# Kernel tuning notes

Hardware: AMD Instinct MI355X
Metric: run time of the kernel (lower is better)

Reference implementation:

```python
import jax, jax.numpy as jnp
import numpy as np

MAX_DIM = 1024
VOCAB = 257
DEPTH = 6
Q_DIM = MAX_DIM // 4  # 256
EXP_DIMS = [1, 2, 4, 8, 16, 32, 64, 128]  # expander sizes: current_q doubles up to Q_DIM
BATCH, SEQ = 8, 4096


def qlinear(q, W):
    """Quaternion Hamilton-product linear.
    q: [..., in, 4] (last dim = r,i,j,k components), W: [4, out, in] (stacked r,i,j,k weights).
    Returns [..., out, 4].
    """
    # P[..., o, w, a] = F.linear(component_a, W_w)  -> all 16 small GEMMs in one einsum
    P = jnp.einsum('...ia,woi->...owa', q, W)
    Pr, Pi, Pj, Pk = P[..., 0, :], P[..., 1, :], P[..., 2, :], P[..., 3, :]  # each [..., out, 4]
    out_r = Pr[..., 0] - Pi[..., 1] - Pj[..., 2] - Pk[..., 3]
    out_i = Pi[..., 0] + Pr[..., 1] + Pk[..., 2] - Pj[..., 3]
    out_j = Pj[..., 0] - Pk[..., 1] + Pr[..., 2] + Pi[..., 3]
    out_k = Pk[..., 0] + Pj[..., 1] - Pi[..., 2] + Pr[..., 3]
    return jnp.stack([out_r, out_i, out_j, out_k], axis=-1)


def qnormalize(q):
    norm = jnp.linalg.norm(q, axis=-1, keepdims=True)
    return q / (norm + 1e-8)


def setup_inputs() -> dict:
    key = jax.random.key(0)
    ks = jax.random.split(key, 4 + len(EXP_DIMS))
    inp = {}
    inp['x'] = jax.random.randint(ks[0], (BATCH, SEQ), 0, VOCAB)
    inp['emb'] = jax.random.normal(ks[1], (VOCAB, 4), dtype=jnp.float32)
    for idx, cq in enumerate(EXP_DIMS):
        scale = cq ** (-0.5)
        inp[f'w_exp{idx}'] = jax.random.uniform(ks[2 + idx], (4, cq, cq), jnp.float32, -scale, scale)
    scale = Q_DIM ** (-0.5)
    inp['w_layers'] = jax.random.uniform(ks[-2], (DEPTH, 4, Q_DIM, Q_DIM), jnp.float32, -scale, scale)
    inp['w_head'] = jax.random.normal(ks[-1], (VOCAB, MAX_DIM), dtype=jnp.float32) * MAX_DIM ** (-0.5)
    return inp


def reference(x, emb, w_exp0, w_exp1, w_exp2, w_exp3, w_exp4, w_exp5, w_exp6, w_exp7,
              w_layers, w_head):
    q = emb[x][:, :, None, :]  # [B, S, 1, 4]
    for w in (w_exp0, w_exp1, w_exp2, w_exp3, w_exp4, w_exp5, w_exp6, w_exp7):
        delta = jnp.tanh(qlinear(q, w))
        q = jnp.concatenate([q + delta, q - delta], axis=2)  # doubles quaternion dim
    for d in range(DEPTH):
        q = qnormalize(qlinear(q, w_layers[d]))
    stability_loss = jnp.mean(jnp.abs(q[..., 0]))
    h_flat = q.reshape(x.shape[0], x.shape[1], -1)  # [B, S, MAX_DIM]
    logits = jnp.einsum('bsd,vd->bsv', h_flat, w_head)
    return (logits, stability_loss)
```

## Files before the change

kernel.cpp:

```cpp
#include <hip/hip_runtime.h>


typedef _Float16 f16x8 __attribute__((ext_vector_type(8)));
typedef float    f32x4 __attribute__((ext_vector_type(4)));

#define GL2LDS16(gp, lp) __builtin_amdgcn_global_load_lds(                     \
    (const __attribute__((address_space(1))) void*)(gp),                       \
    (__attribute__((address_space(3))) void*)(lp), 16, 0, 0)

__device__ __forceinline__ unsigned short f2h(float f) {
  union { _Float16 h; unsigned short u; } c;
  c.h = (_Float16)f;
  return c.u;
}
__device__ __forceinline__ float h2f(unsigned short u) {
  union { unsigned short u; _Float16 h; } c;
  c.u = u;
  return (float)c.h;
}

__global__ __launch_bounds__(256) void expand_ham(
    const float* __restrict__ w, unsigned short* __restrict__ out,
    int cq, int kbits, int total) {
  int id = blockIdx.x * 256 + threadIdx.x;
  if (id >= total) return;
  const int K = 1 << kbits;
  const int n = id >> kbits;
  const int k = id & (K - 1);
  float val = 0.f;
  if (n < 4 * cq) {
    const int o = n >> 2, a = n & 3, i = k >> 2, b = k & 3;
    const int   comp[4][4] = {{0,1,2,3},{1,0,3,2},{2,3,0,1},{3,2,1,0}};
    const float sgn [4][4] = {{1.f,-1.f,-1.f,-1.f},{1.f,1.f,1.f,-1.f},
                              {1.f,-1.f,1.f,1.f},{1.f,1.f,-1.f,1.f}};
    val = sgn[a][b] * w[comp[a][b] * cq * cq + o * cq + i];
  }
  out[id] = f2h(val);
}

__global__ __launch_bounds__(256) void conv_head(
    const float* __restrict__ wh, unsigned short* __restrict__ out) {
  int id = blockIdx.x * 256 + threadIdx.x;
  int v = id >> 10, k = id & 1023;
  out[id] = f2h(v < 257 ? wh[v * 1024 + k] : 0.f);
}

template <int CQ>
__device__ __forceinline__ void exp_step(float (&q)[16][4],
                                         const float* __restrict__ w) {
  float d[CQ][4];
#pragma unroll
  for (int o = 0; o < CQ; o++) {
    float pr = 0.f, pi = 0.f, pj = 0.f, pk = 0.f;
#pragma unroll
    for (int i = 0; i < CQ; i++) {
      const float wr = w[0 * CQ * CQ + o * CQ + i];
      const float wi = w[1 * CQ * CQ + o * CQ + i];
      const float wj = w[2 * CQ * CQ + o * CQ + i];
      const float wk = w[3 * CQ * CQ + o * CQ + i];
      const float qr = q[i][0], qi = q[i][1], qj = q[i][2], qk = q[i][3];
      pr += wr * qr - wi * qi - wj * qj - wk * qk;
      pi += wi * qr + wr * qi + wk * qj - wj * qk;
      pj += wj * qr - wk * qi + wr * qj + wi * qk;
      pk += wk * qr + wj * qi - wi * qj + wr * qk;
    }
    d[o][0] = tanhf(pr); d[o][1] = tanhf(pi);
    d[o][2] = tanhf(pj); d[o][3] = tanhf(pk);
  }
#pragma unroll
  for (int o = 0; o < CQ; o++)
#pragma unroll
    for (int a = 0; a < 4; a++) {
      const float dd = d[o][a], qq = q[o][a];
      q[o][a]      = qq + dd;
      q[CQ + o][a] = qq - dd;
    }
}

__global__ __launch_bounds__(256) void embed_expand(
    const int* __restrict__ x, const float* __restrict__ emb,
    const float* __restrict__ w0, const float* __restrict__ w1,
    const float* __restrict__ w2, const float* __restrict__ w3,
    unsigned short* __restrict__ out) {
  const int t = blockIdx.x * 256 + threadIdx.x;
  float q[16][4];
  const int v = x[t];
  const float4 e = *(const float4*)(emb + v * 4);
  q[0][0] = e.x; q[0][1] = e.y; q[0][2] = e.z; q[0][3] = e.w;
  exp_step<1>(q, w0);
  exp_step<2>(q, w1);
  exp_step<4>(q, w2);
  exp_step<8>(q, w3);
  ushort4* o4 = (ushort4*)(out + (size_t)t * 64);
#pragma unroll
  for (int c = 0; c < 16; c++) {
    ushort4 u;
    u.x = f2h(q[c][0]); u.y = f2h(q[c][1]);
    u.z = f2h(q[c][2]); u.w = f2h(q[c][3]);
    o4[c] = u;
  }
}

template <int EPI>
__global__ __launch_bounds__(256) void gemm_epi(
    const unsigned short* __restrict__ W,
    const unsigned short* __restrict__ Act,
    unsigned short* __restrict__ OutB, float* __restrict__ OutF,
    int K, int Nreal, int ldout) {
  __shared__ unsigned short WtL[128 * 32];
  __shared__ unsigned short WtH[128 * 32];
  __shared__ unsigned short AtL[128 * 32];
  __shared__ unsigned short AtH[128 * 32];

  const int tid  = threadIdx.x;
  const int wave = tid >> 6;
  const int lane = tid & 63;
  const int l15  = lane & 15;
  const int quad = lane >> 4;

  const int Gx = gridDim.x;
  const int L  = blockIdx.y * Gx + blockIdx.x;
  const int j  = L & 7;
  const int s  = L >> 3;
  const int nblock = (s % Gx) * 128;
  const int mblock = (32 * j + s / Gx) * 128;
  const int wn = (wave & 1) * 64;
  const int wm = (wave >> 1) * 64;

  f32x4 acc[4][4];
  const f32x4 zero = {0.f, 0.f, 0.f, 0.f};
#pragma unroll
  for (int a = 0; a < 4; a++)
#pragma unroll
    for (int b = 0; b < 4; b++) acc[a][b] = zero;

  const int row0 = tid >> 2;
  const int sub  = tid & 3;
  const unsigned short* gW0 = W   + (size_t)(nblock + row0)      * K + sub * 8;
  const unsigned short* gW1 = W   + (size_t)(nblock + row0 + 64) * K + sub * 8;
  const unsigned short* gA0 = Act + (size_t)(mblock + row0)      * K + sub * 8;
  const unsigned short* gA1 = Act + (size_t)(mblock + row0 + 64) * K + sub * 8;
  unsigned short* lWL0 = &WtL[wave * 512];
  unsigned short* lWL1 = &WtL[2048 + wave * 512];
  unsigned short* lWH0 = &WtH[wave * 512];
  unsigned short* lWH1 = &WtH[2048 + wave * 512];
  unsigned short* lAL0 = &AtL[wave * 512];
  unsigned short* lAL1 = &AtL[2048 + wave * 512];
  unsigned short* lAH0 = &AtH[wave * 512];
  unsigned short* lAH1 = &AtH[2048 + wave * 512];

  for (int kb = 0; kb < K; kb += 64) {
    GL2LDS16(gW0 + kb,      lWL0);
    GL2LDS16(gW1 + kb,      lWL1);
    GL2LDS16(gW0 + kb + 32, lWH0);
    GL2LDS16(gW1 + kb + 32, lWH1);
    GL2LDS16(gA0 + kb,      lAL0);
    GL2LDS16(gA1 + kb,      lAL1);
    GL2LDS16(gA0 + kb + 32, lAH0);
    GL2LDS16(gA1 + kb + 32, lAH1);
    __syncthreads();

    {
      f16x8 afr[4], bfr[4];
#pragma unroll
      for (int tn = 0; tn < 4; tn++)
        afr[tn] = *(const f16x8*)&WtL[(wn + tn * 16 + l15) * 32 + quad * 8];
#pragma unroll
      for (int tm = 0; tm < 4; tm++)
        bfr[tm] = *(const f16x8*)&AtL[(wm + tm * 16 + l15) * 32 + quad * 8];
#pragma unroll
      for (int tn = 0; tn < 4; tn++)
#pragma unroll
        for (int tm = 0; tm < 4; tm++)
          acc[tn][tm] = __builtin_amdgcn_mfma_f32_16x16x32_f16(
              afr[tn], bfr[tm], acc[tn][tm], 0, 0, 0);
    }
    {
      f16x8 afr[4], bfr[4];
#pragma unroll
      for (int tn = 0; tn < 4; tn++)
        afr[tn] = *(const f16x8*)&WtH[(wn + tn * 16 + l15) * 32 + quad * 8];
#pragma unroll
      for (int tm = 0; tm < 4; tm++)
        bfr[tm] = *(const f16x8*)&AtH[(wm + tm * 16 + l15) * 32 + quad * 8];
#pragma unroll
      for (int tn = 0; tn < 4; tn++)
#pragma unroll
        for (int tm = 0; tm < 4; tm++)
          acc[tn][tm] = __builtin_amdgcn_mfma_f32_16x16x32_f16(
              afr[tn], bfr[tm], acc[tn][tm], 0, 0, 0);
    }
    __syncthreads();
  }

#pragma unroll
  for (int tn = 0; tn < 4; tn++) {
    const int n = nblock + wn + tn * 16 + quad * 4;
    if (n < Nreal) {
#pragma unroll
      for (int tm = 0; tm < 4; tm++) {
        const int token = mblock + wm + tm * 16 + l15;
        const f32x4 v = acc[tn][tm];
        const unsigned short* ip = Act + (size_t)token * K + n;
        const float i0 = h2f(ip[0]), i1 = h2f(ip[1]);
        const float i2 = h2f(ip[2]), i3 = h2f(ip[3]);
        const float d0 = tanhf(v[0]), d1 = tanhf(v[1]);
        const float d2 = tanhf(v[2]), d3 = tanhf(v[3]);
        ushort4 up, um;
        up.x = f2h(i0 + d0); up.y = f2h(i1 + d1);
        up.z = f2h(i2 + d2); up.w = f2h(i3 + d3);
        um.x = f2h(i0 - d0); um.y = f2h(i1 - d1);
        um.z = f2h(i2 - d2); um.w = f2h(i3 - d3);
        *(ushort4*)&OutB[(size_t)token * ldout + n] = up;
        *(ushort4*)&OutB[(size_t)token * ldout + Nreal + n] = um;
      }
    }
  }
}

template <int EPI>
__global__ __launch_bounds__(512, 2) void gemm8p(
    const unsigned short* __restrict__ W,
    const unsigned short* __restrict__ Act,
    unsigned short* __restrict__ OutB, float* __restrict__ OutF,
    int K, int NW, int ldout) {
  __shared__ unsigned short S[65536];
  __shared__ float lsum[8];

  const int tid  = threadIdx.x;
  const int wave = tid >> 6;
  const int lane = tid & 63;
  const int l15  = lane & 15;
  const int quad = lane >> 4;
  const int wr   = wave >> 2;
  const int wc   = wave & 3;

  const int Gx = gridDim.x;
  const int L  = blockIdx.y * Gx + blockIdx.x;
  const int j  = L & 7;
  const int s  = L >> 3;
  const int mtile = j * (gridDim.y >> 3) + s / Gx;
  const int ntile = s % Gx;
  const int nblock = ntile * 256;
  const int mblock = mtile * 256;

  const int NT = K >> 5;

  f32x4 acc[8][4];
  const f32x4 zero = {0.f, 0.f, 0.f, 0.f};
#pragma unroll
  for (int a = 0; a < 8; a++)
#pragma unroll
    for (int b = 0; b < 4; b++) acc[a][b] = zero;

  const int rA = tid >> 2;
  const int sl = (tid & 3) ^ ((tid >> 3) & 3);
  const int w0r = nblock + rA;
  const int w1r = nblock + 128 + rA;
  const int cw0 = w0r < NW ? w0r : NW - 1;
  const int cw1 = w1r < NW ? w1r : NW - 1;
  const unsigned short* sW0 = W   + (size_t)cw0 * K + sl * 8;
  const unsigned short* sW1 = W   + (size_t)cw1 * K + sl * 8;
  const unsigned short* sA0 = Act + (size_t)(mblock + rA)       * K + sl * 8;
  const unsigned short* sA1 = Act + (size_t)(mblock + 128 + rA) * K + sl * 8;

  const int swz = (quad * 8) ^ ((l15 & 6) << 2);

  for (int t = 0; t < 3 && t < NT; ++t) {
    const int kb = t * 32;
    unsigned short* d = S + t * 16384 + tid * 8;
    GL2LDS16(sW0 + kb, d);
    GL2LDS16(sA0 + kb, d + 8192);
    GL2LDS16(sW1 + kb, d + 4096);
    GL2LDS16(sA1 + kb, d + 12288);
  }
  if (NT >= 3)      asm volatile("s_waitcnt vmcnt(8)" ::: "memory");
  else if (NT == 2) asm volatile("s_waitcnt vmcnt(4)" ::: "memory");
  else              asm volatile("s_waitcnt vmcnt(0)" ::: "memory");
  __builtin_amdgcn_s_barrier();
  __builtin_amdgcn_sched_barrier(0);

  for (int kt = 0; kt < NT; ++kt) {
    const unsigned short* SA = S + (kt & 3) * 16384;
    const unsigned short* SB = SA + 8192;
    const int  nxt = (kt + 3) & 3;
    const bool pf  = (kt + 3) < NT;
    const int  kb  = (kt + 3) * 32;
    unsigned short* d = S + nxt * 16384 + tid * 8;

    if (pf) { GL2LDS16(sW0 + kb, d); GL2LDS16(sA0 + kb, d + 8192); }

    f16x8 af[4], bf[4];
#pragma unroll
    for (int t4 = 0; t4 < 4; t4++)
      bf[t4] = *(const f16x8*)(SB + (wc * 64 + t4 * 16 + l15) * 32 + swz);
#pragma unroll
    for (int t4 = 0; t4 < 4; t4++)
      af[t4] = *(const f16x8*)(SA + (wr * 128 + t4 * 16 + l15) * 32 + swz);
    __builtin_amdgcn_s_setprio(1);
#pragma unroll
    for (int tn = 0; tn < 4; tn++)
#pragma unroll
      for (int tm = 0; tm < 4; tm++)
        acc[tn][tm] = __builtin_amdgcn_mfma_f32_16x16x32_f16(
            af[tn], bf[tm], acc[tn][tm], 0, 0, 0);
    __builtin_amdgcn_s_setprio(0);

    if (pf) { GL2LDS16(sW1 + kb, d + 4096); GL2LDS16(sA1 + kb, d + 12288); }

    f16x8 ah[4];
#pragma unroll
    for (int t4 = 0; t4 < 4; t4++)
      ah[t4] = *(const f16x8*)(SA + (wr * 128 + 64 + t4 * 16 + l15) * 32 + swz);
    __builtin_amdgcn_s_setprio(1);
#pragma unroll
    for (int tn = 0; tn < 4; tn++)
#pragma unroll
      for (int tm = 0; tm < 4; tm++)
        acc[4 + tn][tm] = __builtin_amdgcn_mfma_f32_16x16x32_f16(
            ah[tn], bf[tm], acc[4 + tn][tm], 0, 0, 0);
    __builtin_amdgcn_s_setprio(0);

    if (kt < NT - 1) {
      if (kt + 3 < NT)       asm volatile("s_waitcnt vmcnt(8)" ::: "memory");
      else if (kt + 3 == NT) asm volatile("s_waitcnt vmcnt(4)" ::: "memory");
      else                   asm volatile("s_waitcnt vmcnt(0)" ::: "memory");
      __builtin_amdgcn_s_barrier();
      __builtin_amdgcn_sched_barrier(0);
    }
  }

  if constexpr (EPI == 0) {
#pragma unroll
    for (int tn = 0; tn < 8; tn++) {
      const int n = nblock + wr * 128 + tn * 16 + quad * 4;
#pragma unroll
      for (int tm = 0; tm < 4; tm++) {
        const int token = mblock + wc * 64 + tm * 16 + l15;
        const f32x4 v = acc[tn][tm];
        const unsigned short* ip = Act + (size_t)token * K + n;
        const float i0 = h2f(ip[0]), i1 = h2f(ip[1]);
        const float i2 = h2f(ip[2]), i3 = h2f(ip[3]);
        const float d0 = tanhf(v[0]), d1 = tanhf(v[1]);
        const float d2 = tanhf(v[2]), d3 = tanhf(v[3]);
        ushort4 up, um;
        up.x = f2h(i0 + d0); up.y = f2h(i1 + d1);
        up.z = f2h(i2 + d2); up.w = f2h(i3 + d3);
        um.x = f2h(i0 - d0); um.y = f2h(i1 - d1);
        um.z = f2h(i2 - d2); um.w = f2h(i3 - d3);
        *(ushort4*)&OutB[(size_t)token * ldout + n] = up;
        *(ushort4*)&OutB[(size_t)token * ldout + NW + n] = um;
      }
    }
  } else if constexpr (EPI == 1 || EPI == 2) {
    float loss = 0.f;
#pragma unroll
    for (int tn = 0; tn < 8; tn++) {
      const int n = nblock + wr * 128 + tn * 16 + quad * 4;
#pragma unroll
      for (int tm = 0; tm < 4; tm++) {
        const int token = mblock + wc * 64 + tm * 16 + l15;
        const f32x4 v = acc[tn][tm];
        const float nrm =
            sqrtf(v[0] * v[0] + v[1] * v[1] + v[2] * v[2] + v[3] * v[3]);
        const float inv = 1.f / (nrm + 1e-8f);
        ushort4 u;
        u.x = f2h(v[0] * inv); u.y = f2h(v[1] * inv);
        u.z = f2h(v[2] * inv); u.w = f2h(v[3] * inv);
        *(ushort4*)&OutB[(size_t)token * 1024 + n] = u;
        if constexpr (EPI == 2) loss += fabsf(v[0] * inv);
      }
    }
    if constexpr (EPI == 2) {
#pragma unroll
      for (int off = 32; off > 0; off >>= 1) loss += __shfl_down(loss, off);
      if (lane == 0) lsum[wave] = loss;
      __syncthreads();
      if (tid == 0) {
        float t = 0.f;
#pragma unroll
        for (int w8 = 0; w8 < 8; w8++) t += lsum[w8];
        atomicAdd(OutF, t * (1.f / 8388608.f));
      }
    }
  } else {
#pragma unroll
    for (int tn = 0; tn < 8; tn++) {
      const int n = nblock + wr * 128 + tn * 16 + quad * 4;
      if (n < 257) {
#pragma unroll
        for (int tm = 0; tm < 4; tm++) {
          const int token = mblock + wc * 64 + tm * 16 + l15;
          const f32x4 v = acc[tn][tm];
#pragma unroll
          for (int r = 0; r < 4; r++)
            if (n + r < 257) OutF[(size_t)token * 257 + n + r] = v[r];
        }
      }
    }
  }
}

extern "C" void kernel_launch(void* const* d_in, const int* in_sizes, int n_in,
                              void* d_out, int out_size, void* d_ws,
                              size_t ws_size, hipStream_t stream) {
  const int*   x    = (const int*)d_in[0];
  const float* emb  = (const float*)d_in[1];
  const float* we0  = (const float*)d_in[2];
  const float* we1  = (const float*)d_in[3];
  const float* we2  = (const float*)d_in[4];
  const float* we3  = (const float*)d_in[5];
  const float* we4  = (const float*)d_in[6];
  const float* we5  = (const float*)d_in[7];
  const float* we6  = (const float*)d_in[8];
  const float* we7  = (const float*)d_in[9];
  const float* wlay = (const float*)d_in[10];
  const float* wh   = (const float*)d_in[11];
  float* out = (float*)d_out;

  char* p = (char*)d_ws;
  auto alloc = [&](size_t bytes) {
    void* r = (void*)p;
    p += (bytes + 255) & ~(size_t)255;
    return r;
  };
  unsigned short* act0 = (unsigned short*)alloc(32768ull * 1024 * 2);
  unsigned short* act1 = (unsigned short*)alloc(32768ull * 1024 * 2);
  unsigned short* E4 = (unsigned short*)alloc(128 * 64 * 2);
  unsigned short* E5 = (unsigned short*)alloc(128 * 128 * 2);
  unsigned short* E6 = (unsigned short*)alloc(256 * 256 * 2);
  unsigned short* E7 = (unsigned short*)alloc(512 * 512 * 2);
  unsigned short* EL = (unsigned short*)alloc(6ull * 1024 * 1024 * 2);
  unsigned short* WH = (unsigned short*)alloc(384 * 1024 * 2);

  hipMemsetAsync(out + 8421376, 0, 4, stream);

  expand_ham<<<dim3(8192 / 256), 256, 0, stream>>>(we4, E4, 16, 6, 128 * 64);
  expand_ham<<<dim3(16384 / 256), 256, 0, stream>>>(we5, E5, 32, 7, 128 * 128);
  expand_ham<<<dim3(65536 / 256), 256, 0, stream>>>(we6, E6, 64, 8, 256 * 256);
  expand_ham<<<dim3(262144 / 256), 256, 0, stream>>>(we7, E7, 128, 9,
                                                     512 * 512);
  for (int d = 0; d < 6; d++)
    expand_ham<<<dim3(1048576 / 256), 256, 0, stream>>>(
        wlay + (size_t)d * 262144, EL + (size_t)d * 1048576, 256, 10, 1048576);
  conv_head<<<dim3(384 * 1024 / 256), 256, 0, stream>>>(wh, WH);

  embed_expand<<<dim3(128), 256, 0, stream>>>(x, emb, we0, we1, we2, we3, act0);

  gemm_epi<0><<<dim3(1, 256), 256, 0, stream>>>(E4, act0, act1, nullptr, 64,
                                                64, 128);
  gemm_epi<0><<<dim3(1, 256), 256, 0, stream>>>(E5, act1, act0, nullptr, 128,
                                                128, 256);
  gemm8p<0><<<dim3(1, 128), 512, 0, stream>>>(E6, act0, act1, nullptr, 256,
                                              256, 512);
  gemm8p<0><<<dim3(2, 128), 512, 0, stream>>>(E7, act1, act0, nullptr, 512,
                                              512, 1024);

  unsigned short* a = act0;
  unsigned short* b = act1;
  for (int d = 0; d < 5; d++) {
    gemm8p<1><<<dim3(4, 128), 512, 0, stream>>>(EL + (size_t)d * 1048576, a, b,
                                                nullptr, 1024, 1024, 1024);
    unsigned short* t = a; a = b; b = t;
  }
  gemm8p<2><<<dim3(4, 128), 512, 0, stream>>>(EL + 5ull * 1048576, a, b,
                                              out + 8421376, 1024, 1024, 1024);
  { unsigned short* t = a; a = b; b = t; }

  gemm8p<3><<<dim3(2, 128), 512, 0, stream>>>(WH, a, nullptr, out, 1024, 384,
                                              0);
}
```

Before: 995.2 us.

## Shrink gemm8p tile to 128x256 with triple-buffered LDS for higher occupancy

The main GEMM kernel's block tile drops from 256x256 to 128 (weight rows) by 256 (tokens), halving the accumulator registers. LDS staging goes from four 256-row stages to three 128+256-row stages (72KB), and launch bounds now request four blocks per CU instead of two. Grid sizes double in the N direction to match, and the head GEMM now uses 3 N-tiles. The aim is more concurrent waves to hide memory and barrier latency, paid for with lower per-block data reuse, more global traffic per FLOP, and an extra barrier per k-step.

```diff
diff --git a/kernel.cpp b/kernel.cpp
--- a/kernel.cpp
+++ b/kernel.cpp
@@ -219,12 +219,12 @@
 }
 
 template <int EPI>
-__global__ __launch_bounds__(512, 2) void gemm8p(
+__global__ __launch_bounds__(512, 4) void gemm8p(
     const unsigned short* __restrict__ W,
     const unsigned short* __restrict__ Act,
     unsigned short* __restrict__ OutB, float* __restrict__ OutF,
     int K, int NW, int ldout) {
-  __shared__ unsigned short S[65536];
+  __shared__ unsigned short S[3 * 12288];
   __shared__ float lsum[8];
 
   const int tid  = threadIdx.x;
@@ -239,64 +239,63 @@
   const int L  = blockIdx.y * Gx + blockIdx.x;
   const int j  = L & 7;
   const int s  = L >> 3;
-  const int mtile = j * (gridDim.y >> 3) + s / Gx;
-  const int ntile = s % Gx;
-  const int nblock = ntile * 256;
-  const int mblock = mtile * 256;
-
+  const int mblock = (j * (gridDim.y >> 3) + s / Gx) * 256;
+  const int nblock = (s % Gx) * 128;
   const int NT = K >> 5;
 
-  f32x4 acc[8][4];
+  f32x4 acc[4][4];
   const f32x4 zero = {0.f, 0.f, 0.f, 0.f};
 #pragma unroll
-  for (int a = 0; a < 8; a++)
+  for (int a = 0; a < 4; a++)
 #pragma unroll
     for (int b = 0; b < 4; b++) acc[a][b] = zero;
 
-  const int rA = tid >> 2;
+  const int rw = tid >> 2;
   const int sl = (tid & 3) ^ ((tid >> 3) & 3);
-  const int w0r = nblock + rA;
-  const int w1r = nblock + 128 + rA;
-  const int cw0 = w0r < NW ? w0r : NW - 1;
-  const int cw1 = w1r < NW ? w1r : NW - 1;
-  const unsigned short* sW0 = W   + (size_t)cw0 * K + sl * 8;
-  const unsigned short* sW1 = W   + (size_t)cw1 * K + sl * 8;
-  const unsigned short* sA0 = Act + (size_t)(mblock + rA)       * K + sl * 8;
-  const unsigned short* sA1 = Act + (size_t)(mblock + 128 + rA) * K + sl * 8;
+  const int wrow = nblock + rw;
+  const int cwr  = wrow < NW ? wrow : NW - 1;
+  const unsigned short* sW  = W   + (size_t)cwr * K + sl * 8;
+  const unsigned short* sB0 = Act + (size_t)(mblock + rw)       * K + sl * 8;
+  const unsigned short* sB1 = Act + (size_t)(mblock + 128 + rw) * K + sl * 8;
 
   const int swz = (quad * 8) ^ ((l15 & 6) << 2);
 
-  for (int t = 0; t < 3 && t < NT; ++t) {
-    const int kb = t * 32;
-    unsigned short* d = S + t * 16384 + tid * 8;
-    GL2LDS16(sW0 + kb, d);
-    GL2LDS16(sA0 + kb, d + 8192);
-    GL2LDS16(sW1 + kb, d + 4096);
-    GL2LDS16(sA1 + kb, d + 12288);
-  }
-  if (NT >= 3)      asm volatile("s_waitcnt vmcnt(8)" ::: "memory");
-  else if (NT == 2) asm volatile("s_waitcnt vmcnt(4)" ::: "memory");
-  else              asm volatile("s_waitcnt vmcnt(0)" ::: "memory");
+#pragma unroll
+  for (int t = 0; t < 2; ++t) {
+    unsigned short* d = S + t * 12288 + tid * 8;
+    GL2LDS16(sW  + t * 32, d);
+    GL2LDS16(sB0 + t * 32, d + 4096);
+    GL2LDS16(sB1 + t * 32, d + 8192);
+  }
+  asm volatile("s_waitcnt vmcnt(3)" ::: "memory");
   __builtin_amdgcn_s_barrier();
   __builtin_amdgcn_sched_barrier(0);
 
+  int bC = 0;
+  int bS = 2;
   for (int kt = 0; kt < NT; ++kt) {
-    const unsigned short* SA = S + (kt & 3) * 16384;
-    const unsigned short* SB = SA + 8192;
-    const int  nxt = (kt + 3) & 3;
-    const bool pf  = (kt + 3) < NT;
-    const int  kb  = (kt + 3) * 32;
-    unsigned short* d = S + nxt * 16384 + tid * 8;
-
-    if (pf) { GL2LDS16(sW0 + kb, d); GL2LDS16(sA0 + kb, d + 8192); }
+    const unsigned short* SA = S + bC * 12288;
+    const unsigned short* SB = SA + 4096;
 
     f16x8 af[4], bf[4];
+#pragma unroll
+    for (int t4 = 0; t4 < 4; t4++)
+      af[t4] = *(const f16x8*)(SA + (wr * 64 + t4 * 16 + l15) * 32 + swz);
 #pragma unroll
     for (int t4 = 0; t4 < 4; t4++)
       bf[t4] = *(const f16x8*)(SB + (wc * 64 + t4 * 16 + l15) * 32 + swz);
-#pragma unroll
-    for (int t4 = 0; t4 < 4; t4++)
-      af[t4] = *(const f16x8*)(SA + (wr * 128 + t4 * 16 + l15) * 32 + swz);
+
+    if (kt + 2 < NT) {
+      const int kb = (kt + 2) * 32;
+      unsigned short* d = S + bS * 12288 + tid * 8;
+      GL2LDS16(sW  + kb, d);
+      GL2LDS16(sB0 + kb, d + 4096);
+      GL2LDS16(sB1 + kb, d + 8192);
+    }
+
+    __builtin_amdgcn_s_barrier();
+    asm volatile("s_waitcnt lgkmcnt(0)" ::: "memory");
+    __builtin_amdgcn_sched_barrier(0);
     __builtin_amdgcn_s_setprio(1);
 #pragma unroll
     for (int tn = 0; tn < 4; tn++)
@@ -306,34 +305,20 @@
             af[tn], bf[tm], acc[tn][tm], 0, 0, 0);
     __builtin_amdgcn_s_setprio(0);
 
-    if (pf) { GL2LDS16(sW1 + kb, d + 4096); GL2LDS16(sA1 + kb, d + 12288); }
-
-    f16x8 ah[4];
-#pragma unroll
-    for (int t4 = 0; t4 < 4; t4++)
-      ah[t4] = *(const f16x8*)(SA + (wr * 128 + 64 + t4 * 16 + l15) * 32 + swz);
-    __builtin_amdgcn_s_setprio(1);
-#pragma unroll
-    for (int tn = 0; tn < 4; tn++)
-#pragma unroll
-      for (int tm = 0; tm < 4; tm++)
-        acc[4 + tn][tm] = __builtin_amdgcn_mfma_f32_16x16x32_f16(
-            ah[tn], bf[tm], acc[4 + tn][tm], 0, 0, 0);
-    __builtin_amdgcn_s_setprio(0);
-
     if (kt < NT - 1) {
-      if (kt + 3 < NT)       asm volatile("s_waitcnt vmcnt(8)" ::: "memory");
-      else if (kt + 3 == NT) asm volatile("s_waitcnt vmcnt(4)" ::: "memory");
-      else                   asm volatile("s_waitcnt vmcnt(0)" ::: "memory");
+      if (kt + 2 < NT) asm volatile("s_waitcnt vmcnt(3)" ::: "memory");
+      else             asm volatile("s_waitcnt vmcnt(0)" ::: "memory");
       __builtin_amdgcn_s_barrier();
       __builtin_amdgcn_sched_barrier(0);
     }
+    bC = bC == 2 ? 0 : bC + 1;
+    bS = bS == 2 ? 0 : bS + 1;
   }
 
   if constexpr (EPI == 0) {
 #pragma unroll
-    for (int tn = 0; tn < 8; tn++) {
-      const int n = nblock + wr * 128 + tn * 16 + quad * 4;
+    for (int tn = 0; tn < 4; tn++) {
+      const int n = nblock + wr * 64 + tn * 16 + quad * 4;
 #pragma unroll
       for (int tm = 0; tm < 4; tm++) {
         const int token = mblock + wc * 64 + tm * 16 + l15;
@@ -355,8 +340,8 @@
   } else if constexpr (EPI == 1 || EPI == 2) {
     float loss = 0.f;
 #pragma unroll
-    for (int tn = 0; tn < 8; tn++) {
-      const int n = nblock + wr * 128 + tn * 16 + quad * 4;
+    for (int tn = 0; tn < 4; tn++) {
+      const int n = nblock + wr * 64 + tn * 16 + quad * 4;
 #pragma unroll
       for (int tm = 0; tm < 4; tm++) {
         const int token = mblock + wc * 64 + tm * 16 + l15;
@@ -385,8 +370,8 @@
     }
   } else {
 #pragma unroll
-    for (int tn = 0; tn < 8; tn++) {
-      const int n = nblock + wr * 128 + tn * 16 + quad * 4;
+    for (int tn = 0; tn < 4; tn++) {
+      const int n = nblock + wr * 64 + tn * 16 + quad * 4;
       if (n < 257) {
 #pragma unroll
         for (int tm = 0; tm < 4; tm++) {
@@ -451,22 +436,22 @@
                                                 64, 128);
   gemm_epi<0><<<dim3(1, 256), 256, 0, stream>>>(E5, act1, act0, nullptr, 128,
                                                 128, 256);
-  gemm8p<0><<<dim3(1, 128), 512, 0, stream>>>(E6, act0, act1, nullptr, 256,
+  gemm8p<0><<<dim3(2, 128), 512, 0, stream>>>(E6, act0, act1, nullptr, 256,
                                               256, 512);
-  gemm8p<0><<<dim3(2, 128), 512, 0, stream>>>(E7, act1, act0, nullptr, 512,
+  gemm8p<0><<<dim3(4, 128), 512, 0, stream>>>(E7, act1, act0, nullptr, 512,
                                               512, 1024);
 
   unsigned short* a = act0;
   unsigned short* b = act1;
   for (int d = 0; d < 5; d++) {
-    gemm8p<1><<<dim3(4, 128), 512, 0, stream>>>(EL + (size_t)d * 1048576, a, b,
+    gemm8p<1><<<dim3(8, 128), 512, 0, stream>>>(EL + (size_t)d * 1048576, a, b,
                                                 nullptr, 1024, 1024, 1024);
     unsigned short* t = a; a = b; b = t;
   }
-  gemm8p<2><<<dim3(4, 128), 512, 0, stream>>>(EL + 5ull * 1048576, a, b,
+  gemm8p<2><<<dim3(8, 128), 512, 0, stream>>>(EL + 5ull * 1048576, a, b,
                                               out + 8421376, 1024, 1024, 1024);
   { unsigned short* t = a; a = b; b = t; }
 
-  gemm8p<3><<<dim3(2, 128), 512, 0, stream>>>(WH, a, nullptr, out, 1024, 384,
+  gemm8p<3><<<dim3(3, 128), 512, 0, stream>>>(WH, a, nullptr, out, 1024, 384,
                                               0);
 }
```

Measured after the change: 832.7 us. 1.2x faster.
